# Performance work log

Measured on AMD Instinct MI355X. Metric: run time of the kernel, lower is better.

## Reference

```python
import jax, jax.numpy as jnp
import numpy as np

B, H, D = 128, 64, 64  # batch, num_heads, head_dim; einsum structure forces seq n == m == D and H == D


def setup_inputs() -> dict:
    rng = jax.random.key(0)
    ks = jax.random.split(rng, 6)
    query = jax.random.normal(ks[0], (B, H, D, D), jnp.float32)
    key = jax.random.normal(ks[1], (B, H, D, D), jnp.float32) * 0.02
    value = jax.random.normal(ks[2], (B, H, D, D), jnp.float32) * 0.02
    memory_key = jax.random.normal(ks[3], (H, D, D), jnp.float32) * 0.02
    memory_norm = jax.random.uniform(ks[4], (H,), jnp.float32)
    memory_value = jax.random.normal(ks[5], (H, D, D), jnp.float32) * 0.02
    compression_rate = jnp.ones((H,), jnp.float32)
    return {"query": query, "key": key, "value": value,
            "memory_key": memory_key, "memory_norm": memory_norm,
            "memory_value": memory_value, "compression_rate": compression_rate}


def reference(query, key, value, memory_key, memory_norm, memory_value, compression_rate):
    h = memory_norm.shape[0]
    d = memory_key.shape[-1]

    # ---- update(key, value): associative binding + running stats (torch no_grad block) ----
    # binding in fp16 then cast to fp32, exactly as the source einsum does
    binding = jnp.einsum('bhnd,bhmd->bhnm',
                         key.astype(jnp.float16),
                         value.astype(jnp.float16)).astype(jnp.float32)
    mean_binding = binding.reshape(-1, h).mean(axis=0)            # [H] (row-major flatten, as torch .view)
    k_flat = key.reshape(-1, h, d)                                # [B*N, H, D]
    v_flat = value.reshape(-1, h, d)
    mean_value = v_flat.mean(axis=0)                              # [H, D]
    mean_key_norm = jnp.linalg.norm(k_flat.mean(axis=0), axis=-1) # [H]
    # source resets memory_key to zeros [H, D] (shape check always fires), then addcmul_
    new_memory_key = mean_binding[:, None] * mean_value           # [H, D]
    new_memory_norm = memory_norm + mean_key_norm                 # [H]
    # conditional adaptive compression
    factor = jnp.where(new_memory_norm.mean() > 0.9, compression_rate,
                       jnp.ones_like(compression_rate))
    new_memory_key = jax.lax.stop_gradient(new_memory_key * factor[:, None])
    new_memory_norm = jax.lax.stop_gradient(new_memory_norm * factor)

    # ---- retrieve(query): normalized linear-attention readout ----
    scores = jnp.einsum('bhnd,hnm->bhmd',
                        query.astype(jnp.float16),
                        memory_key.astype(jnp.float16)).astype(jnp.float32)
    # source broadcasts memory_norm [H] over the trailing dim (valid since H == D)
    scores = scores / (memory_norm + 1e-6)
    memory_output = jnp.einsum('bhmd,hnm->bhnd', scores, memory_value)
    return memory_output, scores, new_memory_key, new_memory_norm
```

## Files before the change

kernel.cpp:

```cpp
#include <hip/hip_runtime.h>
#include <hip/hip_fp16.h>

typedef _Float16 f16x8 __attribute__((ext_vector_type(8)));
typedef _Float16 f16x4 __attribute__((ext_vector_type(4)));
typedef float f32x4 __attribute__((ext_vector_type(4)));

__device__ __forceinline__ f32x4 ntld4(const float* p) {
    return __builtin_nontemporal_load((const f32x4*)p);
}
__device__ __forceinline__ float ntld1(const float* p) {
    return __builtin_nontemporal_load(p);
}
__device__ __forceinline__ f32x4 ld4(const float* p) {
    return *(const f32x4*)p;
}
__device__ __forceinline__ void ntst4(float* p, f32x4 v) {
    __builtin_nontemporal_store(v, (f32x4*)p);
}

__global__ __launch_bounds__(256) void mega(
    const float* __restrict__ q,   const float* __restrict__ key,
    const float* __restrict__ val, const float* __restrict__ mk,
    const float* __restrict__ mnorm, const float* __restrict__ mv,
    float* __restrict__ out_mo, float* __restrict__ out_sc,
    float* __restrict__ skp, float* __restrict__ svp, float* __restrict__ pbp,
    const int nbR)
{
    __shared__ union SM {
        struct { _Float16 qT[64][72]; _Float16 mkT[64][72]; } f;
        struct { float ktile[64][68]; float red[256]; float ks[64]; } r;
    } sm;

    const int t   = threadIdx.x;
    const int bid = blockIdx.x;

    if (bid < nbR) {
        const int r0 = t >> 4;
        const int c0 = (t & 15) << 2;
        f32x4 ska[4] = {}; f32x4 sva[4] = {};
        float pba[4] = {0.f, 0.f, 0.f, 0.f};
        f32x4 ka[4], va[4];
        int i = bid;
#pragma unroll
        for (int qq = 0; qq < 4; ++qq) {
            const int row = r0 + 16 * qq;
            ka[qq] = ntld4(key + (size_t)i * 4096 + row * 64 + c0);
            va[qq] = ntld4(val + (size_t)i * 4096 + row * 64 + c0);
        }
        while (true) {
            const int inx = i + nbR;
            const bool more = (inx < 8192);
            f32x4 kn4[4], vn4[4];
            if (more) {
#pragma unroll
                for (int qq = 0; qq < 4; ++qq) {
                    const int row = r0 + 16 * qq;
                    kn4[qq] = ntld4(key + (size_t)inx * 4096 + row * 64 + c0);
                    vn4[qq] = ntld4(val + (size_t)inx * 4096 + row * 64 + c0);
                }
            }
#pragma unroll
            for (int qq = 0; qq < 4; ++qq) {
                const int row = r0 + 16 * qq;
                ska[qq] += ka[qq];
                sva[qq] += va[qq];
                *(f32x4*)&sm.r.ktile[row][c0] = ka[qq];
            }
            __syncthreads();
            {
                const int d  = t & 63;
                const int rr = (t >> 6) * 16;
                float p = 0.f;
#pragma unroll
                for (int r = 0; r < 16; ++r) p += sm.r.ktile[rr + r][d];
                sm.r.red[t] = p;
            }
            __syncthreads();
            if (t < 64)
                sm.r.ks[t] = sm.r.red[t] + sm.r.red[t + 64] + sm.r.red[t + 128] + sm.r.red[t + 192];
            __syncthreads();
#pragma unroll
            for (int qq = 0; qq < 4; ++qq) {
                float pq = va[qq][0] * sm.r.ks[c0]     + va[qq][1] * sm.r.ks[c0 + 1]
                         + va[qq][2] * sm.r.ks[c0 + 2] + va[qq][3] * sm.r.ks[c0 + 3];
                pq += __shfl_xor(pq, 1);
                pq += __shfl_xor(pq, 2);
                pq += __shfl_xor(pq, 4);
                pq += __shfl_xor(pq, 8);
                pba[qq] += pq;
            }
            if (!more) break;
#pragma unroll
            for (int qq = 0; qq < 4; ++qq) { ka[qq] = kn4[qq]; va[qq] = vn4[qq]; }
            i = inx;
        }
        const size_t pb4 = (size_t)bid * 4096;
#pragma unroll
        for (int qq = 0; qq < 4; ++qq) {
            ntst4(skp + pb4 + 4 * t + 1024 * qq, ska[qq]);
            ntst4(svp + pb4 + 4 * t + 1024 * qq, sva[qq]);
        }
        if ((t & 15) == 0) {
#pragma unroll
            for (int qq = 0; qq < 4; ++qq)
                pbp[bid * 64 + r0 + 16 * qq] = pba[qq];
        }
        return;
    }

    const int fid = bid - nbR;
    const int h   = fid >> 7;
    const int b   = fid & 127;
    const int bh  = b * 64 + h;
    const float* qb  = q  + (size_t)bh * 4096;
    const float* mkb = mk + h * 4096;
    const float* mvb = mv + h * 4096;

    const int w  = t >> 6;
    const int l  = t & 63;
    const int lr = l & 15;
    const int lk = l >> 4;
    const size_t gbase = (size_t)bh * 4096;

    {
        const int d  = t & 63;
        const int n0 = (t >> 6) * 16;
#pragma unroll
        for (int half = 0; half < 2; ++half) {
            const int nh = n0 + 8 * half;
            float qv[8], kv[8];
#pragma unroll
            for (int i = 0; i < 8; ++i) qv[i] = ntld1(qb + (nh + i) * 64 + d);
#pragma unroll
            for (int i = 0; i < 8; ++i) kv[i] = mkb[(nh + i) * 64 + d];
            f16x8 qh, kh;
#pragma unroll
            for (int i = 0; i < 8; ++i) { qh[i] = (_Float16)qv[i]; kh[i] = (_Float16)kv[i]; }
            *(f16x8*)&sm.f.qT [d][nh] = qh;
            *(f16x8*)&sm.f.mkT[d][nh] = kh;
        }
    }
    __syncthreads();

    f32x4 acc[4] = {};
#pragma unroll
    for (int kn = 0; kn < 2; ++kn) {
        f16x8 bfr = *(const f16x8*)&sm.f.mkT[16 * w + lr][kn * 32 + lk * 8];
#pragma unroll
        for (int di = 0; di < 4; ++di) {
            f16x8 afr = *(const f16x8*)&sm.f.qT[16 * di + lr][kn * 32 + lk * 8];
            acc[di] = __builtin_amdgcn_mfma_f32_16x16x32_f16(afr, bfr, acc[di], 0, 0, 0);
        }
    }
    __syncthreads();

    f32x4 mva[4];
    {
        const float* rowp = mvb + (16 * w + lr) * 64 + lk * 8;
        mva[0] = ld4(rowp);      mva[1] = ld4(rowp + 4);
        mva[2] = ld4(rowp + 32); mva[3] = ld4(rowp + 36);
    }

    _Float16* sT = &sm.f.qT[0][0];
    const int m = 16 * w + lr;
#pragma unroll
    for (int di = 0; di < 4; ++di) {
        const int d0 = 16 * di + 4 * lk;
        f32x4 nv = ld4(mnorm + d0);
        f32x4 sv;
#pragma unroll
        for (int r = 0; r < 4; ++r) {
            sv[r] = acc[di][r] * __builtin_amdgcn_rcpf(nv[r] + 1e-6f);
            sT[(d0 + r) * 72 + m] = (_Float16)sv[r];
        }
        ntst4(out_sc + gbase + (size_t)m * 64 + d0, sv);
    }
    __syncthreads();

    f16x8 b2[2];
#pragma unroll
    for (int kn = 0; kn < 2; ++kn) {
        f16x8 vv;
#pragma unroll
        for (int j = 0; j < 4; ++j) {
            vv[j]     = (_Float16)mva[2 * kn][j];
            vv[j + 4] = (_Float16)mva[2 * kn + 1][j];
        }
        b2[kn] = vv;
    }
    f32x4 acc2[4] = {};
#pragma unroll
    for (int kn = 0; kn < 2; ++kn) {
#pragma unroll
        for (int di = 0; di < 4; ++di) {
            f16x8 afr = *(const f16x8*)(sT + (16 * di + lr) * 72 + kn * 32 + lk * 8);
            acc2[di] = __builtin_amdgcn_mfma_f32_16x16x32_f16(afr, b2[kn], acc2[di], 0, 0, 0);
        }
    }
#pragma unroll
    for (int di = 0; di < 4; ++di) {
        const int d0 = 16 * di + 4 * lk;
        f32x4 ov;
#pragma unroll
        for (int r = 0; r < 4; ++r) ov[r] = acc2[di][r];
        ntst4(out_mo + gbase + (size_t)m * 64 + d0, ov);
    }
}

#define NCHUNK 8
__global__ __launch_bounds__(256) void reduce2(
    const float* __restrict__ skp, const float* __restrict__ svp,
    const float* __restrict__ pbp, float* __restrict__ p2,
    const int nbR, const int clen)
{
    const int bi = blockIdx.x;
    const int c  = bi / 33;
    const int e  = (bi % 33) * 256 + threadIdx.x;
    if (e >= 8256) return;
    int n0 = c * clen;
    int n1 = n0 + clen; if (n1 > nbR) n1 = nbR;
    float s = 0.f;
    if (e < 4096) {
        for (int n = n0; n < n1; ++n) s += skp[(size_t)n * 4096 + e];
    } else if (e < 8192) {
        const int e2 = e - 4096;
        for (int n = n0; n < n1; ++n) s += svp[(size_t)n * 4096 + e2];
    } else {
        const int e2 = e - 8192;
        for (int n = n0; n < n1; ++n) s += pbp[n * 64 + e2];
    }
    p2[c * 8256 + e] = s;
}

__global__ __launch_bounds__(256) void finalize(
    const float* __restrict__ p2, const float* __restrict__ mnorm,
    const float* __restrict__ crate,
    float* __restrict__ out_nmk, float* __restrict__ out_nmn)
{
    __shared__ float tot[8256];
    __shared__ float fac_s[64];
    const int t = threadIdx.x;
    for (int e = t; e < 8256; e += 256) {
        float s = 0.f;
#pragma unroll
        for (int c = 0; c < NCHUNK; ++c) s += p2[c * 8256 + e];
        tot[e] = s;
    }
    __syncthreads();
    const float* sk_tot = tot;
    const float* sv_tot = tot + 4096;
    const float* pb_tot = tot + 8192;
    if (t < 64) {
        float ss = 0.f;
#pragma unroll 8
        for (int dd = 0; dd < 64; ++dd) {
            float mkm = sk_tot[t * 64 + dd] * (1.0f / 8192.0f);
            ss += mkm * mkm;
        }
        const float nmn = mnorm[t] + sqrtf(ss);
        float v = nmn;
        for (int off = 32; off; off >>= 1) v += __shfl_xor(v, off);
        const float mean = v * (1.0f / 64.0f);
        const float f = (mean > 0.9f) ? crate[t] : 1.0f;
        fac_s[t] = f;
        out_nmn[t] = nmn * f;
    }
    __syncthreads();
    for (int e = t; e < 4096; e += 256) {
        const int jh = e >> 6;
        const float mb = pb_tot[jh] * (1.0f / 524288.0f);
        const float mvv = sv_tot[e] * (1.0f / 8192.0f);
        out_nmk[e] = mb * mvv * fac_s[jh];
    }
}

extern "C" void kernel_launch(void* const* d_in, const int* in_sizes, int n_in,
                              void* d_out, int out_size, void* d_ws, size_t ws_size,
                              hipStream_t stream) {
    const float* q  = (const float*)d_in[0];
    const float* k  = (const float*)d_in[1];
    const float* v  = (const float*)d_in[2];
    const float* mk = (const float*)d_in[3];
    const float* mn = (const float*)d_in[4];
    const float* mv = (const float*)d_in[5];
    const float* cr = (const float*)d_in[6];

    float* out     = (float*)d_out;
    float* out_mo  = out;
    float* out_sc  = out + 33554432;
    float* out_nmk = out + 67108864;
    float* out_nmn = out + 67112960;

    float* ws   = (float*)d_ws;
    float* p2   = ws;
    float* part = ws + NCHUNK * 8256;
    const size_t wsf = ws_size / 4;
    const size_t used = NCHUNK * 8256;
    const size_t avail = (wsf > used) ? (wsf - used) : 0;
    int nb = (int)(avail / 8256);
    if (nb > 256) nb = 256;
    if (nb < 1)   nb = 1;
    float* skp = part;
    float* svp = part + (size_t)nb * 4096;
    float* pbp = svp  + (size_t)nb * 4096;
    const int clen = (nb + NCHUNK - 1) / NCHUNK;

    hipLaunchKernelGGL(mega, dim3(nb + 8192), dim3(256), 0, stream,
                       q, k, v, mk, mn, mv, out_mo, out_sc, skp, svp, pbp, nb);
    hipLaunchKernelGGL(reduce2, dim3(33 * NCHUNK), dim3(256), 0, stream,
                       skp, svp, pbp, p2, nb, clen);
    hipLaunchKernelGGL(finalize, dim3(1), dim3(256), 0, stream,
                       p2, mn, cr, out_nmk, out_nmn);
}
```

Before: 164.8 us.

## Precompute per-head fused memory matrix to collapse two GEMMs into one pass

Adds a prep kernel that, for each head, converts memory_key to a transposed fp16 layout and precomputes W = memory_value·memory_key in fp16. The main kernel then computes scores and memory_output from the same query fragment in a single MFMA loop, applying the norm scaling to both results afterwards. This removes the second GEMM stage, the LDS round-trip of scores, two barriers and the per-block fp32 loads and conversions of the memory matrices. In exchange it changes rounding: the output no longer passes through fp16-rounded scores, it adds an extra kernel launch, and it uses more workspace, which reduces the number of reduction partial blocks.

```diff
diff --git a/kernel.cpp b/kernel.cpp
--- a/kernel.cpp
+++ b/kernel.cpp
@@ -2,7 +2,6 @@
 #include <hip/hip_fp16.h>
 
 typedef _Float16 f16x8 __attribute__((ext_vector_type(8)));
-typedef _Float16 f16x4 __attribute__((ext_vector_type(4)));
 typedef float f32x4 __attribute__((ext_vector_type(4)));
 
 __device__ __forceinline__ f32x4 ntld4(const float* p) {
@@ -18,16 +17,72 @@
     __builtin_nontemporal_store(v, (f32x4*)p);
 }
 
+__global__ __launch_bounds__(256) void prep(
+    const float* __restrict__ mk, const float* __restrict__ mv,
+    _Float16* __restrict__ mkTb, _Float16* __restrict__ Wb)
+{
+    __shared__ _Float16 mks[64][72];
+    __shared__ _Float16 mvs[64][72];
+    const int t = threadIdx.x;
+    const int h = blockIdx.x;
+    const float* mkb = mk + h * 4096;
+    const float* mvb = mv + h * 4096;
+    {
+        const int nn = t >> 2, m0 = (t & 3) * 16;
+        f32x4 a0 = ld4(mkb + nn * 64 + m0),     a1 = ld4(mkb + nn * 64 + m0 + 4);
+        f32x4 a2 = ld4(mkb + nn * 64 + m0 + 8), a3 = ld4(mkb + nn * 64 + m0 + 12);
+        f32x4 b0 = ld4(mvb + nn * 64 + m0),     b1 = ld4(mvb + nn * 64 + m0 + 4);
+        f32x4 b2 = ld4(mvb + nn * 64 + m0 + 8), b3 = ld4(mvb + nn * 64 + m0 + 12);
+        f16x8 k0, k1, v0, v1;
+#pragma unroll
+        for (int i = 0; i < 4; ++i) {
+            k0[i] = (_Float16)a0[i]; k0[i + 4] = (_Float16)a1[i];
+            k1[i] = (_Float16)a2[i]; k1[i + 4] = (_Float16)a3[i];
+            v0[i] = (_Float16)b0[i]; v0[i + 4] = (_Float16)b1[i];
+            v1[i] = (_Float16)b2[i]; v1[i + 4] = (_Float16)b3[i];
+        }
+        *(f16x8*)&mks[nn][m0]     = k0;
+        *(f16x8*)&mks[nn][m0 + 8] = k1;
+        *(f16x8*)&mvs[nn][m0]     = v0;
+        *(f16x8*)&mvs[nn][m0 + 8] = v1;
+    }
+    __syncthreads();
+    const int w = t >> 6, l = t & 63, lr = l & 15, lk = l >> 4;
+    f32x4 acc[4] = {};
+#pragma unroll
+    for (int kn = 0; kn < 2; ++kn) {
+        f16x8 bfr = *(const f16x8*)&mks[16 * w + lr][kn * 32 + lk * 8];
+#pragma unroll
+        for (int di = 0; di < 4; ++di) {
+            f16x8 afr = *(const f16x8*)&mvs[16 * di + lr][kn * 32 + lk * 8];
+            acc[di] = __builtin_amdgcn_mfma_f32_16x16x32_f16(afr, bfr, acc[di], 0, 0, 0);
+        }
+    }
+#pragma unroll
+    for (int di = 0; di < 4; ++di)
+#pragma unroll
+        for (int r = 0; r < 4; ++r)
+            Wb[h * 4096 + (16 * di + 4 * lk + r) * 64 + 16 * w + lr] = (_Float16)acc[di][r];
+    {
+        const int m = t & 63, n0 = (t >> 6) * 16;
+        f16x8 x0, x1;
+#pragma unroll
+        for (int i = 0; i < 8; ++i) { x0[i] = mks[n0 + i][m]; x1[i] = mks[n0 + 8 + i][m]; }
+        *(f16x8*)&mkTb[h * 4096 + m * 64 + n0]     = x0;
+        *(f16x8*)&mkTb[h * 4096 + m * 64 + n0 + 8] = x1;
+    }
+}
+
 __global__ __launch_bounds__(256) void mega(
     const float* __restrict__ q,   const float* __restrict__ key,
-    const float* __restrict__ val, const float* __restrict__ mk,
-    const float* __restrict__ mnorm, const float* __restrict__ mv,
+    const float* __restrict__ val, const _Float16* __restrict__ mkTb,
+    const float* __restrict__ mnorm, const _Float16* __restrict__ Wb,
     float* __restrict__ out_mo, float* __restrict__ out_sc,
     float* __restrict__ skp, float* __restrict__ svp, float* __restrict__ pbp,
     const int nbR)
 {
     __shared__ union SM {
-        struct { _Float16 qT[64][72]; _Float16 mkT[64][72]; } f;
+        struct { _Float16 qT[64][72]; } f;
         struct { float ktile[64][68]; float red[256]; float ks[64]; } r;
     } sm;
 
@@ -112,97 +167,67 @@
     const int h   = fid >> 7;
     const int b   = fid & 127;
     const int bh  = b * 64 + h;
-    const float* qb  = q  + (size_t)bh * 4096;
-    const float* mkb = mk + h * 4096;
-    const float* mvb = mv + h * 4096;
+    const float* qb = q + (size_t)bh * 4096;
 
     const int w  = t >> 6;
     const int l  = t & 63;
     const int lr = l & 15;
     const int lk = l >> 4;
-    const size_t gbase = (size_t)bh * 4096;
+
+    f16x8 bfrK[2], bfrW[2];
+    {
+        const _Float16* mrow = mkTb + h * 4096 + (16 * w + lr) * 64 + lk * 8;
+        const _Float16* wrow = Wb   + h * 4096 + (16 * w + lr) * 64 + lk * 8;
+        bfrK[0] = *(const f16x8*)(mrow);
+        bfrK[1] = *(const f16x8*)(mrow + 32);
+        bfrW[0] = *(const f16x8*)(wrow);
+        bfrW[1] = *(const f16x8*)(wrow + 32);
+    }
+    f32x4 scl[4];
+#pragma unroll
+    for (int di = 0; di < 4; ++di) {
+        f32x4 nv = ld4(mnorm + 16 * di + 4 * lk);
+#pragma unroll
+        for (int r = 0; r < 4; ++r) scl[di][r] = __builtin_amdgcn_rcpf(nv[r] + 1e-6f);
+    }
 
     {
         const int d  = t & 63;
         const int n0 = (t >> 6) * 16;
-#pragma unroll
-        for (int half = 0; half < 2; ++half) {
-            const int nh = n0 + 8 * half;
-            float qv[8], kv[8];
-#pragma unroll
-            for (int i = 0; i < 8; ++i) qv[i] = ntld1(qb + (nh + i) * 64 + d);
-#pragma unroll
-            for (int i = 0; i < 8; ++i) kv[i] = mkb[(nh + i) * 64 + d];
-            f16x8 qh, kh;
-#pragma unroll
-            for (int i = 0; i < 8; ++i) { qh[i] = (_Float16)qv[i]; kh[i] = (_Float16)kv[i]; }
-            *(f16x8*)&sm.f.qT [d][nh] = qh;
-            *(f16x8*)&sm.f.mkT[d][nh] = kh;
-        }
+        float qv[16];
+#pragma unroll
+        for (int i = 0; i < 16; ++i) qv[i] = ntld1(qb + (n0 + i) * 64 + d);
+        f16x8 qh0, qh1;
+#pragma unroll
+        for (int i = 0; i < 8; ++i) { qh0[i] = (_Float16)qv[i]; qh1[i] = (_Float16)qv[i + 8]; }
+        *(f16x8*)&sm.f.qT[d][n0]     = qh0;
+        *(f16x8*)&sm.f.qT[d][n0 + 8] = qh1;
     }
     __syncthreads();
 
-    f32x4 acc[4] = {};
+    f32x4 accS[4] = {}, accO[4] = {};
 #pragma unroll
     for (int kn = 0; kn < 2; ++kn) {
-        f16x8 bfr = *(const f16x8*)&sm.f.mkT[16 * w + lr][kn * 32 + lk * 8];
 #pragma unroll
         for (int di = 0; di < 4; ++di) {
             f16x8 afr = *(const f16x8*)&sm.f.qT[16 * di + lr][kn * 32 + lk * 8];
-            acc[di] = __builtin_amdgcn_mfma_f32_16x16x32_f16(afr, bfr, acc[di], 0, 0, 0);
-        }
-    }
-    __syncthreads();
-
-    f32x4 mva[4];
-    {
-        const float* rowp = mvb + (16 * w + lr) * 64 + lk * 8;
-        mva[0] = ld4(rowp);      mva[1] = ld4(rowp + 4);
-        mva[2] = ld4(rowp + 32); mva[3] = ld4(rowp + 36);
-    }
-
-    _Float16* sT = &sm.f.qT[0][0];
+            accS[di] = __builtin_amdgcn_mfma_f32_16x16x32_f16(afr, bfrK[kn], accS[di], 0, 0, 0);
+            accO[di] = __builtin_amdgcn_mfma_f32_16x16x32_f16(afr, bfrW[kn], accO[di], 0, 0, 0);
+        }
+    }
+
     const int m = 16 * w + lr;
+    const size_t gbase = (size_t)bh * 4096;
 #pragma unroll
     for (int di = 0; di < 4; ++di) {
         const int d0 = 16 * di + 4 * lk;
-        f32x4 nv = ld4(mnorm + d0);
-        f32x4 sv;
+        f32x4 sv, ov;
 #pragma unroll
         for (int r = 0; r < 4; ++r) {
-            sv[r] = acc[di][r] * __builtin_amdgcn_rcpf(nv[r] + 1e-6f);
-            sT[(d0 + r) * 72 + m] = (_Float16)sv[r];
+            sv[r] = accS[di][r] * scl[di][r];
+            ov[r] = accO[di][r] * scl[di][r];
         }
         ntst4(out_sc + gbase + (size_t)m * 64 + d0, sv);
-    }
-    __syncthreads();
-
-    f16x8 b2[2];
-#pragma unroll
-    for (int kn = 0; kn < 2; ++kn) {
-        f16x8 vv;
-#pragma unroll
-        for (int j = 0; j < 4; ++j) {
-            vv[j]     = (_Float16)mva[2 * kn][j];
-            vv[j + 4] = (_Float16)mva[2 * kn + 1][j];
-        }
-        b2[kn] = vv;
-    }
-    f32x4 acc2[4] = {};
-#pragma unroll
-    for (int kn = 0; kn < 2; ++kn) {
-#pragma unroll
-        for (int di = 0; di < 4; ++di) {
-            f16x8 afr = *(const f16x8*)(sT + (16 * di + lr) * 72 + kn * 32 + lk * 8);
-            acc2[di] = __builtin_amdgcn_mfma_f32_16x16x32_f16(afr, b2[kn], acc2[di], 0, 0, 0);
-        }
-    }
-#pragma unroll
-    for (int di = 0; di < 4; ++di) {
-        const int d0 = 16 * di + 4 * lk;
-        f32x4 ov;
-#pragma unroll
-        for (int r = 0; r < 4; ++r) ov[r] = acc2[di][r];
         ntst4(out_mo + gbase + (size_t)m * 64 + d0, ov);
     }
 }
@@ -293,9 +318,11 @@
 
     float* ws   = (float*)d_ws;
     float* p2   = ws;
-    float* part = ws + NCHUNK * 8256;
+    _Float16* mkTb = (_Float16*)(ws + NCHUNK * 8256);
+    _Float16* Wb   = mkTb + 64 * 4096;
+    float* part = ws + NCHUNK * 8256 + 262144;
     const size_t wsf = ws_size / 4;
-    const size_t used = NCHUNK * 8256;
+    const size_t used = NCHUNK * 8256 + 262144;
     const size_t avail = (wsf > used) ? (wsf - used) : 0;
     int nb = (int)(avail / 8256);
     if (nb > 256) nb = 256;
@@ -305,8 +332,10 @@
     float* pbp = svp  + (size_t)nb * 4096;
     const int clen = (nb + NCHUNK - 1) / NCHUNK;
 
+    hipLaunchKernelGGL(prep, dim3(64), dim3(256), 0, stream,
+                       mk, mv, mkTb, Wb);
     hipLaunchKernelGGL(mega, dim3(nb + 8192), dim3(256), 0, stream,
-                       q, k, v, mk, mn, mv, out_mo, out_sc, skp, svp, pbp, nb);
+                       q, k, v, mkTb, mn, Wb, out_mo, out_sc, skp, svp, pbp, nb);
     hipLaunchKernelGGL(reduce2, dim3(33 * NCHUNK), dim3(256), 0, stream,
                        skp, svp, pbp, p2, nb, clen);
     hipLaunchKernelGGL(finalize, dim3(1), dim3(256), 0, stream,
```

Result: slower. 174.6 us (+6.0%).
